# Kernel tuning notes

Measured on AMD Instinct MI355X. Metric: run time of the kernel, lower is better.

The kernel has to match this reference:

```python
import jax, jax.numpy as jnp
import numpy as np

EMBED_DIM = 1024
Q_HEADS = 16
KV_HEADS = 8            # n_heads // 2 per CrossAttention
HEAD_DIM = EMBED_DIM // Q_HEADS   # 64
KV_EMBED = HEAD_DIM * KV_HEADS    # 512
GROUPS = Q_HEADS // KV_HEADS      # 2
LN_EPS = 1e-5
RMS_EPS = 1e-6


def _rms_norm(x):
    # SimpleRMSNorm (no learned scale) used inside BitLinear
    return x * jax.lax.rsqrt(jnp.mean(jnp.square(x), axis=-1, keepdims=True) + RMS_EPS)


def _act_quant(x):
    # per-token 8-bit absmax activation quant (BitNet b1.58)
    scale = 127.0 / jnp.maximum(jnp.max(jnp.abs(x), axis=-1, keepdims=True), 1e-5)
    return jnp.clip(jnp.round(x * scale), -128.0, 127.0) / scale


def _weight_quant(w):
    # ternary {-1,0,1} absmean weight quant
    scale = 1.0 / jnp.maximum(jnp.mean(jnp.abs(w)), 1e-5)
    return jnp.clip(jnp.round(w * scale), -1.0, 1.0) / scale


def _ste(a, q):
    # straight-through estimator: forward=q, backward=identity
    return a + jax.lax.stop_gradient(q - a)


def bit_linear(x, w):
    # x: [b, n, in], w: [out, in] (torch Linear layout), no bias
    xn = _rms_norm(x)
    xq = _ste(xn, _act_quant(xn))
    wq = _ste(w, _weight_quant(w))
    return jnp.einsum('bni,oi->bno', xq, wq)


def setup_inputs() -> dict:
    key = jax.random.key(0)
    ks = jax.random.split(key, 6)
    B, N, S, D = 16, 1024, 256, EMBED_DIM
    s = D ** -0.5
    return {
        'x': jax.random.normal(ks[0], (B, N, D), jnp.float32),
        'y': jax.random.normal(ks[1], (B, S, D), jnp.float32),
        'wq': jax.random.normal(ks[2], (D, D), jnp.float32) * s,
        'wk': jax.random.normal(ks[3], (KV_EMBED, D), jnp.float32) * s,
        'wv': jax.random.normal(ks[4], (KV_EMBED, D), jnp.float32) * s,
        'wo': jax.random.normal(ks[5], (D, D), jnp.float32) * s,
        'ln_gamma': jnp.ones((D,), jnp.float32),
        'ln_beta': jnp.zeros((D,), jnp.float32),
    }


def reference(x, y, wq, wk, wv, wo, ln_gamma, ln_beta):
    B, N, D = x.shape
    S = y.shape[1]
    # ternary-quantized projections
    q = bit_linear(x, wq).reshape(B, N, Q_HEADS, HEAD_DIM)
    k = bit_linear(y, wk).reshape(B, S, KV_HEADS, HEAD_DIM)
    v = bit_linear(y, wv).reshape(B, S, KV_HEADS, HEAD_DIM)
    # grouped-query attention: split q heads as (kv_head, group)
    q = jnp.transpose(q, (0, 2, 1, 3)) / (HEAD_DIM ** 0.5)   # [b, Hq, n, d]
    q = q.reshape(B, KV_HEADS, GROUPS, N, HEAD_DIM)           # [b, h, g, n, d]
    k = jnp.transpose(k, (0, 2, 1, 3))                        # [b, h, s, d]
    v = jnp.transpose(v, (0, 2, 1, 3))
    scores = jnp.einsum('bhgnd,bhsd->bhgns', q, k)
    attn = jax.nn.softmax(scores, axis=-1)                    # is_causal=False, no mask
    out = jnp.einsum('bhgns,bhsd->bhgnd', attn, v)
    out = jnp.transpose(out, (0, 3, 1, 2, 4)).reshape(B, N, D)  # b n (h g) d -> b n D
    # LayerNorm before out projection
    mu = jnp.mean(out, axis=-1, keepdims=True)
    var = jnp.mean(jnp.square(out - mu), axis=-1, keepdims=True)
    out = (out - mu) * jax.lax.rsqrt(var + LN_EPS) * ln_gamma + ln_beta
    return bit_linear(out, wo)
```

## Files before the change

kernel.cpp:

```cpp
#include <hip/hip_runtime.h>
#include <hip/hip_bf16.h>

typedef int int4v __attribute__((ext_vector_type(4)));
typedef float float4v __attribute__((ext_vector_type(4)));
typedef _Float16 half8 __attribute__((ext_vector_type(8)));

#define DEV __device__ __forceinline__

DEV signed char quant8(float v) {
    int q = (int)rintf(v);
    q = q < -128 ? -128 : (q > 127 ? 127 : q);
    return (signed char)q;
}

DEV int tern1(float v) {
    int q = (int)rintf(v);
    q = q < -1 ? -1 : (q > 1 ? 1 : q);
    return q;
}

DEV void gl2lds16(const void* g, void* l) {
    __builtin_amdgcn_global_load_lds(
        (const __attribute__((address_space(1))) void*)g,
        (__attribute__((address_space(3))) void*)l, 16, 0, 0);
}

DEV float beta_of(const double* __restrict__ part, int wi) {
    int offs = wi == 0 ? 0 : (wi == 1 ? 64 : (wi == 2 ? 96 : 128));
    int cnt  = (wi == 1 || wi == 2) ? 32 : 64;
    double invc = (wi == 1 || wi == 2) ? (1.0 / 524288.0) : (1.0 / 1048576.0);
    int lane = threadIdx.x & 63;
    double v = (lane < cnt) ? part[offs + lane] : 0.0;
    #pragma unroll
    for (int o = 32; o > 0; o >>= 1) v += __shfl_down(v, o);
    v = __shfl(v, 0);
    return fmaxf((float)(v * invc), 1e-5f);
}

__global__ __launch_bounds__(256) void absmean_all(
    const float* __restrict__ WQ, const float* __restrict__ WK,
    const float* __restrict__ WV, const float* __restrict__ WO,
    double* __restrict__ part)
{
    __shared__ double red[256];
    int bx = blockIdx.x, t = threadIdx.x;
    const float* W; int rel;
    if (bx < 64)       { W = WQ; rel = bx; }
    else if (bx < 96)  { W = WK; rel = bx - 64; }
    else if (bx < 128) { W = WV; rel = bx - 96; }
    else               { W = WO; rel = bx - 128; }
    size_t base = (size_t)rel * 16384;
    double acc = 0.0;
    for (int i = t; i < 16384; i += 256) acc += (double)fabsf(W[base + i]);
    red[t] = acc; __syncthreads();
    #pragma unroll
    for (int o = 128; o > 0; o >>= 1) {
        if (t < o) red[t] += red[t + o];
        __syncthreads();
    }
    if (t == 0) part[bx] = red[0];
}

DEV void act_row(const float* __restrict__ X, signed char* __restrict__ X8,
                 float* __restrict__ RS, int blk)
{
    int row = blk * 4 + (threadIdx.x >> 6);
    int lane = threadIdx.x & 63;
    const float4* xr = (const float4*)(X + (size_t)row * 1024) + lane * 4;
    float4 u[4];
    #pragma unroll
    for (int i = 0; i < 4; i++) u[i] = xr[i];
    float ss = 0.f, am = 0.f;
    #pragma unroll
    for (int i = 0; i < 4; i++) {
        ss += u[i].x * u[i].x + u[i].y * u[i].y + u[i].z * u[i].z + u[i].w * u[i].w;
        am = fmaxf(am, fmaxf(fmaxf(fabsf(u[i].x), fabsf(u[i].y)),
                             fmaxf(fabsf(u[i].z), fabsf(u[i].w))));
    }
    #pragma unroll
    for (int o = 32; o > 0; o >>= 1) {
        ss += __shfl_xor(ss, o);
        am = fmaxf(am, __shfl_xor(am, o));
    }
    float r = 1.f / sqrtf(ss * (1.f / 1024.f) + 1e-6f);
    float m = fmaxf(am * r, 1e-5f);
    float s = 127.f / m;
    int pk[4];
    #pragma unroll
    for (int i = 0; i < 4; i++) {
        int q0 = quant8((u[i].x * r) * s);
        int q1 = quant8((u[i].y * r) * s);
        int q2 = quant8((u[i].z * r) * s);
        int q3 = quant8((u[i].w * r) * s);
        pk[i] = (q0 & 0xff) | ((q1 & 0xff) << 8) | ((q2 & 0xff) << 16) | ((q3 & 0xff) << 24);
    }
    int4v pv = {pk[0], pk[1], pk[2], pk[3]};
    ((int4v*)(X8 + (size_t)row * 1024))[lane] = pv;
    if (lane == 0) RS[row] = m * (1.f / 127.f);
}

__global__ __launch_bounds__(256) void prep_all(
    const float* __restrict__ WQ, const float* __restrict__ WK,
    const float* __restrict__ WV, const float* __restrict__ WO,
    signed char* __restrict__ w8, const double* __restrict__ part,
    const float* __restrict__ X, signed char* __restrict__ X8, float* __restrict__ XS,
    const float* __restrict__ Y, signed char* __restrict__ Y8, float* __restrict__ YS)
{
    int bx = blockIdx.x;
    if (bx < 3072) {
        const float* W; signed char* O; int rel, wi;
        if (bx < 1024)      { W = WQ; O = w8;                           rel = bx;        wi = 0; }
        else if (bx < 1536) { W = WK; O = w8 + (1 << 20);               rel = bx - 1024; wi = 1; }
        else if (bx < 2048) { W = WV; O = w8 + (1 << 20) + (512 << 10); rel = bx - 1536; wi = 2; }
        else                { W = WO; O = w8 + (2 << 20);               rel = bx - 2048; wi = 3; }
        float inv = 1.f / beta_of(part, wi);
        int i = rel * 256 + threadIdx.x;
        float4 u = ((const float4*)W)[i];
        int q0 = tern1(u.x * inv);
        int q1 = tern1(u.y * inv);
        int q2 = tern1(u.z * inv);
        int q3 = tern1(u.w * inv);
        int packed = (q0 & 0xff) | ((q1 & 0xff) << 8) | ((q2 & 0xff) << 16) | ((q3 & 0xff) << 24);
        ((int*)O)[i] = packed;
    } else if (bx < 7168) {
        act_row(X, X8, XS, bx - 3072);
    } else {
        act_row(Y, Y8, YS, bx - 7168);
    }
}

DEV void gemm_core(
    signed char* As0, signed char* Bs0, signed char* As1, signed char* Bs1,
    const signed char* __restrict__ A, const signed char* __restrict__ B,
    float* __restrict__ outF, _Float16* __restrict__ outH,
    _Float16* __restrict__ outK, _Float16* __restrict__ outV,
    int N, int K,
    const float* __restrict__ rowscale, const double* __restrict__ part,
    int b0i, int b1i, int split, float extra, int mode,
    int bM, int bN)
{
    const int tid = threadIdx.x;
    const int lane = tid & 63, wid = tid >> 6;
    const int wr = wid >> 1, wc = wid & 1;
    const int lr = lane & 15, quad = lane >> 4;

    int4v zero = {0, 0, 0, 0};
    int4v acc[4][4];
    #pragma unroll
    for (int i = 0; i < 4; i++)
        #pragma unroll
        for (int j = 0; j < 4; j++) acc[i][j] = zero;

    const int srow = wid * 32 + (lane >> 2);
    const int soff = (lane & 3) * 16;
    const signed char* gA0 = A + (size_t)(bM * 128 + srow) * K + soff;
    const signed char* gA1 = gA0 + (size_t)16 * K;
    const signed char* gB0 = B + (size_t)(bN * 128 + srow) * K + soff;
    const signed char* gB1 = gB0 + (size_t)16 * K;
    const int lo0 = wid * 2048, lo1 = wid * 2048 + 1024;

    gl2lds16(gA0, As0 + lo0);
    gl2lds16(gA1, As0 + lo1);
    gl2lds16(gB0, Bs0 + lo0);
    gl2lds16(gB1, Bs0 + lo1);
    const float s0 = beta_of(part, b0i) * extra;
    const float s1 = (b1i == b0i) ? s0 : beta_of(part, b1i) * extra;
    __syncthreads();

#define GEMM_COMPUTE(AS, BS)                                                   \
    {                                                                          \
        int4v af[4], bfr[4];                                                   \
        _Pragma("unroll")                                                      \
        for (int tm = 0; tm < 4; tm++)                                         \
            af[tm] = *(const int4v*)((AS) + (wr * 64 + tm * 16 + lr) * 64 + quad * 16); \
        _Pragma("unroll")                                                      \
        for (int tn = 0; tn < 4; tn++)                                         \
            bfr[tn] = *(const int4v*)((BS) + (wc * 64 + tn * 16 + lr) * 64 + quad * 16); \
        _Pragma("unroll")                                                      \
        for (int tm = 0; tm < 4; tm++)                                         \
            _Pragma("unroll")                                                  \
            for (int tn = 0; tn < 4; tn++)                                     \
                acc[tm][tn] = __builtin_amdgcn_mfma_i32_16x16x64_i8(af[tm], bfr[tn], acc[tm][tn], 0, 0, 0); \
    }

    for (int kb = 0; kb < K; kb += 128) {
        if (kb + 64 < K) {
            gl2lds16(gA0 + kb + 64, As1 + lo0);
            gl2lds16(gA1 + kb + 64, As1 + lo1);
            gl2lds16(gB0 + kb + 64, Bs1 + lo0);
            gl2lds16(gB1 + kb + 64, Bs1 + lo1);
        }
        GEMM_COMPUTE(As0, Bs0);
        __syncthreads();
        if (kb + 128 < K) {
            gl2lds16(gA0 + kb + 128, As0 + lo0);
            gl2lds16(gA1 + kb + 128, As0 + lo1);
            gl2lds16(gB0 + kb + 128, Bs0 + lo0);
            gl2lds16(gB1 + kb + 128, Bs0 + lo1);
        }
        GEMM_COMPUTE(As1, Bs1);
        __syncthreads();
    }
#undef GEMM_COMPUTE

    #pragma unroll
    for (int tm = 0; tm < 4; tm++) {
        #pragma unroll
        for (int r = 0; r < 4; r++) {
            int grow = bM * 128 + wr * 64 + tm * 16 + quad * 4 + r;
            float rs = rowscale[grow];
            #pragma unroll
            for (int tn = 0; tn < 4; tn++) {
                int col = bN * 128 + wc * 64 + tn * 16 + lr;
                float v = (float)acc[tm][tn][r] * rs * (col < split ? s0 : s1);
                if (mode == 0) {
                    outF[(size_t)grow * N + col] = v;
                } else if (mode == 1) {
                    outH[(size_t)grow * 1024 + col] = (_Float16)v;
                } else {
                    if (col < 512)
                        outK[(size_t)grow * 512 + col] = (_Float16)v;
                    else
                        outV[((size_t)(grow >> 8) * 512 + (col - 512)) * 256 + (grow & 255)] = (_Float16)v;
                }
            }
        }
    }
}

__global__ __launch_bounds__(256) void proj_fused(
    const signed char* __restrict__ x8, const signed char* __restrict__ wq8,
    const signed char* __restrict__ y8, const signed char* __restrict__ kv8,
    _Float16* __restrict__ qf16, _Float16* __restrict__ kf16,
    _Float16* __restrict__ vt16,
    const float* __restrict__ xs, const float* __restrict__ ys,
    const double* __restrict__ part)
{
    __shared__ __align__(16) signed char As0[128 * 64 + 8192];
    __shared__ __align__(16) signed char Bs0[128 * 64];
    __shared__ __align__(16) signed char As1[128 * 64];
    __shared__ __align__(16) signed char Bs1[128 * 64];
    const int b = blockIdx.x;
    const int x = b & 7, s = b >> 3;
    if (s < 128) {
        int qi = x * 128 + s;
        gemm_core(As0, Bs0, As1, Bs1, x8, wq8, nullptr, qf16, nullptr, nullptr,
                  1024, 1024, xs, part, 0, 0, 1024, 0.125f, 1, qi >> 3, qi & 7);
    } else {
        int ki = x * 32 + (s - 128);
        gemm_core(As0, Bs0, As1, Bs1, y8, kv8, nullptr, nullptr, kf16, vt16,
                  1024, 1024, ys, part, 1, 2, 512, 1.f, 2, ki >> 3, ki & 7);
    }
}

__global__ __launch_bounds__(256) void gemm_out(
    const signed char* __restrict__ A, const signed char* __restrict__ B,
    float* __restrict__ outF,
    const float* __restrict__ rowscale, const double* __restrict__ part)
{
    __shared__ __align__(16) signed char As0[128 * 64];
    __shared__ __align__(16) signed char Bs0[128 * 64];
    __shared__ __align__(16) signed char As1[128 * 64];
    __shared__ __align__(16) signed char Bs1[128 * 64];
    const int flat = blockIdx.y * 8 + blockIdx.x;
    const int chunk = (gridDim.x * gridDim.y) >> 3;
    const int f2 = (flat & 7) * chunk + (flat >> 3);
    gemm_core(As0, Bs0, As1, Bs1, A, B, outF, nullptr, nullptr, nullptr,
              1024, 1024, rowscale, part, 3, 3, 1024, 1.f, 0, f2 >> 3, f2 & 7);
}

__global__ __launch_bounds__(256, 4) void attn_mfma(
    const _Float16* Qh, const _Float16* __restrict__ Kh,
    const _Float16* __restrict__ Vt, _Float16* Oh)
{
    __shared__ __align__(16) _Float16 KVs[256 * 64];

    const int tid = threadIdx.x;
    const int lane = tid & 63;
    const int w = tid >> 6;
    const int lq = lane & 15;
    const int quad = lane >> 4;
    const int swz = (lq & 7) << 4;

    const int bx = blockIdx.x;
    const int nt = bx & 15, g = (bx >> 4) & 1, h = (bx >> 5) & 7, b = bx >> 8;
    const int rbase = b * 1024 + nt * 64 + w * 16;
    const int qcol0 = (h * 2 + g) * 64;

    half8 aq[2];
    #pragma unroll
    for (int ks = 0; ks < 2; ks++)
        aq[ks] = *(const half8*)(Qh + (size_t)(rbase + lq) * 1024 + qcol0 + ks * 32 + quad * 8);

    {
        int kb = tid >> 3;
        int c  = tid & 7;
        int rp = (kb & 3) | ((kb >> 1) & 12) | ((kb & 4) << 2);
        const _Float16* kg = Kh + (size_t)(b * 256 + kb) * 512 + h * 64 + c * 8;
        char* lb = (char*)KVs;
        #pragma unroll
        for (int j = 0; j < 8; j++) {
            int row = 32 * j + rp;
            int off = (row * 128 + c * 16) ^ ((row & 7) << 4);
            *(half8*)(lb + off) = *(const half8*)(kg + (size_t)32 * j * 512);
        }
    }
    __syncthreads();

    float4v acc[16];
    float4v zf = {0.f, 0.f, 0.f, 0.f};
    #pragma unroll
    for (int t = 0; t < 16; t++) acc[t] = zf;
    const int kc0 = (quad * 16) ^ swz;
    const int kc1 = (64 + quad * 16) ^ swz;
    __builtin_amdgcn_s_setprio(1);
    #pragma unroll
    for (int t = 0; t < 16; t++) {
        const char* krow = (const char*)KVs + (t * 16 + lq) * 128;
        half8 kf0 = *(const half8*)(krow + kc0);
        acc[t] = __builtin_amdgcn_mfma_f32_16x16x32_f16(kf0, aq[0], acc[t], 0, 0, 0);
        half8 kf1 = *(const half8*)(krow + kc1);
        acc[t] = __builtin_amdgcn_mfma_f32_16x16x32_f16(kf1, aq[1], acc[t], 0, 0, 0);
    }
    __builtin_amdgcn_s_setprio(0);

    float m = acc[0][0];
    #pragma unroll
    for (int t = 0; t < 16; t++) {
        #pragma unroll
        for (int r = 0; r < 4; r++) m = fmaxf(m, acc[t][r]);
    }
    m = fmaxf(m, __shfl_xor(m, 16));
    m = fmaxf(m, __shfl_xor(m, 32));
    float l = 0.f;
    #pragma unroll
    for (int t = 0; t < 16; t++) {
        #pragma unroll
        for (int r = 0; r < 4; r++) {
            float p = __expf(acc[t][r] - m);
            acc[t][r] = p;
            l += p;
        }
    }
    l += __shfl_xor(l, 16);
    l += __shfl_xor(l, 32);

    __syncthreads();

    {
        int row = tid >> 5, c = tid & 31;
        const _Float16* vg = Vt + ((size_t)b * 512 + h * 64 + row) * 256 + c * 8;
        char* lb = (char*)KVs;
        #pragma unroll
        for (int j = 0; j < 8; j++) {
            int rr = row + 8 * j;
            int off = (rr * 512 + c * 16) ^ ((rr & 7) << 4);
            *(half8*)(lb + off) = *(const half8*)(vg + (size_t)8 * j * 256);
        }
    }
    __syncthreads();

    float4v oacc[4];
    #pragma unroll
    for (int dt = 0; dt < 4; dt++) oacc[dt] = zf;
    __builtin_amdgcn_s_setprio(1);
    #pragma unroll
    for (int ks = 0; ks < 8; ks++) {
        half8 pf;
        #pragma unroll
        for (int r = 0; r < 4; r++) {
            pf[r]     = (_Float16)acc[2 * ks][r];
            pf[4 + r] = (_Float16)acc[2 * ks + 1][r];
        }
        const int vc = (ks * 64 + quad * 16) ^ swz;
        #pragma unroll
        for (int dt = 0; dt < 4; dt++) {
            half8 bv = *(const half8*)((const char*)KVs + (dt * 16 + lq) * 512 + vc);
            oacc[dt] = __builtin_amdgcn_mfma_f32_16x16x32_f16(pf, bv, oacc[dt], 0, 0, 0);
        }
    }
    __builtin_amdgcn_s_setprio(0);

    float linv = 1.f / l;
    float invr[4];
    #pragma unroll
    for (int r = 0; r < 4; r++) invr[r] = __shfl(linv, quad * 4 + r);
    #pragma unroll
    for (int dt = 0; dt < 4; dt++) {
        #pragma unroll
        for (int r = 0; r < 4; r++) {
            Oh[(size_t)(rbase + quad * 4 + r) * 1024 + qcol0 + dt * 16 + lq] =
                (_Float16)(oacc[dt][r] * invr[r]);
        }
    }
}

__global__ __launch_bounds__(256) void ln_quant(
    const _Float16* __restrict__ AO, const float* __restrict__ G,
    const float* __restrict__ Bt, signed char* __restrict__ O8,
    float* __restrict__ OS)
{
    int row = blockIdx.x * 4 + (threadIdx.x >> 6);
    int lane = threadIdx.x & 63;
    const _Float16* xr = AO + (size_t)row * 1024 + lane * 16;
    half8 h0 = *(const half8*)xr;
    half8 h1 = *(const half8*)(xr + 8);
    float x[16];
    #pragma unroll
    for (int i = 0; i < 8; i++) { x[i] = (float)h0[i]; x[8 + i] = (float)h1[i]; }
    float sx = 0.f, sx2 = 0.f;
    #pragma unroll
    for (int i = 0; i < 16; i++) { sx += x[i]; sx2 += x[i] * x[i]; }
    #pragma unroll
    for (int o = 32; o > 0; o >>= 1) {
        sx += __shfl_xor(sx, o);
        sx2 += __shfl_xor(sx2, o);
    }
    float mu = sx * (1.f / 1024.f);
    float var = sx2 * (1.f / 1024.f) - mu * mu;
    float rstd = 1.f / sqrtf(var + 1e-5f);

    const float4* gp = (const float4*)(G + lane * 16);
    const float4* bp = (const float4*)(Bt + lane * 16);
    float l[16];
    #pragma unroll
    for (int i = 0; i < 4; i++) {
        float4 gv = gp[i], bv = bp[i];
        l[i * 4 + 0] = (x[i * 4 + 0] - mu) * rstd * gv.x + bv.x;
        l[i * 4 + 1] = (x[i * 4 + 1] - mu) * rstd * gv.y + bv.y;
        l[i * 4 + 2] = (x[i * 4 + 2] - mu) * rstd * gv.z + bv.z;
        l[i * 4 + 3] = (x[i * 4 + 3] - mu) * rstd * gv.w + bv.w;
    }
    float msq = 0.f, am = 0.f;
    #pragma unroll
    for (int i = 0; i < 16; i++) { msq += l[i] * l[i]; am = fmaxf(am, fabsf(l[i])); }
    #pragma unroll
    for (int o = 32; o > 0; o >>= 1) {
        msq += __shfl_xor(msq, o);
        am = fmaxf(am, __shfl_xor(am, o));
    }
    float r2 = 1.f / sqrtf(msq * (1.f / 1024.f) + 1e-6f);
    float mx = fmaxf(am * r2, 1e-5f);
    float s = 127.f / mx;
    int pk[4];
    #pragma unroll
    for (int i = 0; i < 4; i++) {
        int q0 = quant8((l[i * 4 + 0] * r2) * s);
        int q1 = quant8((l[i * 4 + 1] * r2) * s);
        int q2 = quant8((l[i * 4 + 2] * r2) * s);
        int q3 = quant8((l[i * 4 + 3] * r2) * s);
        pk[i] = (q0 & 0xff) | ((q1 & 0xff) << 8) | ((q2 & 0xff) << 16) | ((q3 & 0xff) << 24);
    }
    int4v pv = {pk[0], pk[1], pk[2], pk[3]};
    ((int4v*)(O8 + (size_t)row * 1024))[lane] = pv;
    if (lane == 0) OS[row] = mx * (1.f / 127.f);
}

extern "C" void kernel_launch(void* const* d_in, const int* in_sizes, int n_in,
                              void* d_out, int out_size, void* d_ws, size_t ws_size,
                              hipStream_t stream)
{
    const float* X  = (const float*)d_in[0];
    const float* Y  = (const float*)d_in[1];
    const float* WQ = (const float*)d_in[2];
    const float* WK = (const float*)d_in[3];
    const float* WV = (const float*)d_in[4];
    const float* WO = (const float*)d_in[5];
    const float* G  = (const float*)d_in[6];
    const float* Bt = (const float*)d_in[7];

    char* ws = (char*)d_ws;
    double* part  = (double*)(ws + 256);
    char* w8  = ws + 4096;
    char* x8  = w8 + (3 << 20);
    char* y8  = x8 + (16 << 20);
    float* xs = (float*)(y8 + (4 << 20));
    float* ys = xs + 16384;
    float* os = ys + 4096;
    _Float16* qf16 = (_Float16*)(os + 16384);
    _Float16* kf16 = qf16 + (size_t)16384 * 1024;
    _Float16* vt16 = kf16 + (size_t)4096 * 512;
    char* wq8 = w8;
    char* kv8 = w8 + (1 << 20);
    char* wo8 = w8 + (2 << 20);
    char* o8  = x8;

    absmean_all<<<192, 256, 0, stream>>>(WQ, WK, WV, WO, part);

    prep_all<<<8192, 256, 0, stream>>>(
        WQ, WK, WV, WO, (signed char*)w8, part,
        X, (signed char*)x8, xs, Y, (signed char*)y8, ys);

    proj_fused<<<1280, 256, 0, stream>>>(
        (signed char*)x8, (signed char*)wq8, (signed char*)y8, (signed char*)kv8,
        qf16, kf16, vt16, xs, ys, part);

    attn_mfma<<<4096, 256, 0, stream>>>(qf16, kf16, vt16, qf16);

    ln_quant<<<4096, 256, 0, stream>>>(qf16, G, Bt, (signed char*)o8, os);

    gemm_out<<<dim3(8, 128), 256, 0, stream>>>(
        (signed char*)o8, (signed char*)wo8, (float*)d_out, os, part);
}
```

Measured before the change: 290.9 us.

## Restructure int8 GEMM K-loop with explicit vmcnt waits and early refill

The int8 MFMA GEMM main loop now prefetches two K-stages up front. Each step waits only for the older stage with s_waitcnt vmcnt(4) plus a raw s_barrier, instead of draining all loads at __syncthreads. After the LDS fragments are read into registers, a second barrier lets the same buffer be refilled with the stage two steps ahead while the MFMAs run. The aim is to keep more global-to-LDS loads in flight and overlap them with compute. It relies on hand-written waitcnt counts that must match the number of outstanding loads, and it uses two barriers per step.

```diff
diff --git a/kernel.cpp b/kernel.cpp
--- a/kernel.cpp
+++ b/kernel.cpp
@@ -24,6 +24,10 @@
         (const __attribute__((address_space(1))) void*)g,
         (__attribute__((address_space(3))) void*)l, 16, 0, 0);
 }
+
+DEV void wait_vm4()   { asm volatile("s_waitcnt vmcnt(4)" ::: "memory"); }
+DEV void wait_vm0()   { asm volatile("s_waitcnt vmcnt(0)" ::: "memory"); }
+DEV void wait_lgkm0() { asm volatile("s_waitcnt lgkmcnt(0)" ::: "memory"); }
 
 DEV float beta_of(const double* __restrict__ part, int wi) {
     int offs = wi == 0 ? 0 : (wi == 1 ? 64 : (wi == 2 ? 96 : 128));
@@ -159,16 +163,23 @@
     const signed char* gB1 = gB0 + (size_t)16 * K;
     const int lo0 = wid * 2048, lo1 = wid * 2048 + 1024;
 
-    gl2lds16(gA0, As0 + lo0);
-    gl2lds16(gA1, As0 + lo1);
-    gl2lds16(gB0, Bs0 + lo0);
-    gl2lds16(gB1, Bs0 + lo1);
+#define STAGE4(AS, BS, kb)                     \
+    do {                                       \
+        gl2lds16(gA0 + (kb), (AS) + lo0);      \
+        gl2lds16(gA1 + (kb), (AS) + lo1);      \
+        gl2lds16(gB0 + (kb), (BS) + lo0);      \
+        gl2lds16(gB1 + (kb), (BS) + lo1);      \
+    } while (0)
+
+    STAGE4(As0, Bs0, 0);
+    STAGE4(As1, Bs1, 64);
     const float s0 = beta_of(part, b0i) * extra;
     const float s1 = (b1i == b0i) ? s0 : beta_of(part, b1i) * extra;
-    __syncthreads();
-
-#define GEMM_COMPUTE(AS, BS)                                                   \
+
+#define GEMM_STEP(AS, BS, LAST, DO_STAGE, KB2)                                 \
     {                                                                          \
+        if (LAST) wait_vm0(); else wait_vm4();                                 \
+        __builtin_amdgcn_s_barrier();                                          \
         int4v af[4], bfr[4];                                                   \
         _Pragma("unroll")                                                      \
         for (int tm = 0; tm < 4; tm++)                                         \
@@ -176,6 +187,10 @@
         _Pragma("unroll")                                                      \
         for (int tn = 0; tn < 4; tn++)                                         \
             bfr[tn] = *(const int4v*)((BS) + (wc * 64 + tn * 16 + lr) * 64 + quad * 16); \
+        wait_lgkm0();                                                          \
+        __builtin_amdgcn_sched_barrier(0);                                     \
+        __builtin_amdgcn_s_barrier();                                          \
+        if (DO_STAGE) STAGE4(AS, BS, KB2);                                     \
         _Pragma("unroll")                                                      \
         for (int tm = 0; tm < 4; tm++)                                         \
             _Pragma("unroll")                                                  \
@@ -184,24 +199,12 @@
     }
 
     for (int kb = 0; kb < K; kb += 128) {
-        if (kb + 64 < K) {
-            gl2lds16(gA0 + kb + 64, As1 + lo0);
-            gl2lds16(gA1 + kb + 64, As1 + lo1);
-            gl2lds16(gB0 + kb + 64, Bs1 + lo0);
-            gl2lds16(gB1 + kb + 64, Bs1 + lo1);
-        }
-        GEMM_COMPUTE(As0, Bs0);
-        __syncthreads();
-        if (kb + 128 < K) {
-            gl2lds16(gA0 + kb + 128, As0 + lo0);
-            gl2lds16(gA1 + kb + 128, As0 + lo1);
-            gl2lds16(gB0 + kb + 128, Bs0 + lo0);
-            gl2lds16(gB1 + kb + 128, Bs0 + lo1);
-        }
-        GEMM_COMPUTE(As1, Bs1);
-        __syncthreads();
-    }
-#undef GEMM_COMPUTE
+        GEMM_STEP(As0, Bs0, (kb + 64 >= K), (kb + 128 < K), kb + 128);
+        if (kb + 64 < K)
+            GEMM_STEP(As1, Bs1, (kb + 128 >= K), (kb + 192 < K), kb + 192);
+    }
+#undef GEMM_STEP
+#undef STAGE4
 
     #pragma unroll
     for (int tm = 0; tm < 4; tm++) {
```

Result: faster. 284.6 us (-2.1%).
